# Kernel tuning notes

Measured on AMD Instinct MI355X. Metric: run time of the kernel, lower is better.

## Reference

```python
import jax, jax.numpy as jnp
import numpy as np

EPS_LN = 1e-5
EPS_W = 1e-16
K = 3


def layernorm(x, gamma, beta):
    mu = x.mean(-1, keepdims=True)
    var = ((x - mu) ** 2).mean(-1, keepdims=True)
    return (x - mu) * jax.lax.rsqrt(var + EPS_LN) * gamma + beta


def knn_interp(xb, pos_x, pos_y, k=K):
    """Inverse-squared-distance kNN interpolation.
    xb: [B, Nx, C] source features; pos_x: [Nx, 3]; pos_y: [Ny, 3].
    Positions are identical across batch (torch code expands them), so the
    kNN search is done once and the gather is broadcast over batch.
    Returns [B, Ny, C]."""
    # squared distances via ||y||^2 + ||x||^2 - 2 y.x  -> [Ny, Nx]
    d2 = ((pos_y * pos_y).sum(-1)[:, None]
          + (pos_x * pos_x).sum(-1)[None, :]
          - 2.0 * pos_y @ pos_x.T)
    _, idx = jax.lax.top_k(-d2, k)                      # [Ny, k] nearest
    # exact squared distances for the selected neighbors (matches torch math)
    diff = pos_x[idx] - pos_y[:, None, :]               # [Ny, k, 3]
    w = 1.0 / jnp.clip((diff * diff).sum(-1), EPS_W)    # [Ny, k]
    xg = xb[:, idx, :]                                  # [B, Ny, k, C]
    num = (xg * w[None, :, :, None]).sum(2)             # [B, Ny, C]
    return num / w.sum(1)[None, :, None]


def setup_inputs() -> dict:
    key = jax.random.key(0)
    k1, k2, k3 = jax.random.split(key, 3)
    B, N_MESH, N_PIV, C = 4, 40000, 2000, 128
    return {
        "node_features": jax.random.normal(k1, (B * N_MESH, C), jnp.float32),
        "gamma": jnp.ones((C,), jnp.float32),
        "beta": jnp.zeros((C,), jnp.float32),
        "position_mesh": jax.random.uniform(k2, (N_MESH, 3), jnp.float32),
        "position_pivotal": jax.random.uniform(k3, (N_PIV, 3), jnp.float32),
        "batch_size": 4,
    }


def reference(node_features, gamma, beta, position_mesh, position_pivotal, batch_size):
    B = batch_size
    C = node_features.shape[-1]
    Nm = position_mesh.shape[0]
    # encode: PivotalNorm then mesh -> pivotal interpolation
    h = layernorm(node_features, gamma, beta)
    hb = h.reshape(B, Nm, C)
    piv = knn_interp(hb, position_mesh, position_pivotal, K)      # [B, Npiv, C]
    # decode: pivotal -> mesh interpolation
    mesh = knn_interp(piv, position_pivotal, position_mesh, K)    # [B, Nm, C]
    return mesh.reshape(B * Nm, C)
```

## Files before the change

### kernel.cpp

```cpp
#include <hip/hip_runtime.h>
#include <hip/hip_bf16.h>
#include <math.h>

#define EPS_LN 1e-5f
#define EPS_W  1e-16f

__device__ __forceinline__ float cvt(const __hip_bfloat16 v) { return __bfloat162float(v); }
__device__ __forceinline__ float cvt(const float v)          { return v; }

__device__ __forceinline__ void load8(const __hip_bfloat16* p, float* x) {
    union { uint4 v; __hip_bfloat16 h[8]; } t;
    t.v = *(const uint4*)p;
    #pragma unroll
    for (int i = 0; i < 8; ++i) x[i] = __bfloat162float(t.h[i]);
}
__device__ __forceinline__ void load8(const float* p, float* x) {
    float4 a = *(const float4*)p, b = *(const float4*)(p + 4);
    x[0]=a.x; x[1]=a.y; x[2]=a.z; x[3]=a.w; x[4]=b.x; x[5]=b.y; x[6]=b.z; x[7]=b.w;
}

__device__ __forceinline__ void ins3lex(float nd, int ni, float d[3], int ix[3]) {
    bool b2 = (nd < d[2]) || (nd == d[2] && ni < ix[2]);
    if (!b2) return;
    bool b1 = (nd < d[1]) || (nd == d[1] && ni < ix[1]);
    bool b0 = (nd < d[0]) || (nd == d[0] && ni < ix[0]);
    if (b0)      { d[2]=d[1]; ix[2]=ix[1]; d[1]=d[0]; ix[1]=ix[0]; d[0]=nd; ix[0]=ni; }
    else if (b1) { d[2]=d[1]; ix[2]=ix[1]; d[1]=nd; ix[1]=ni; }
    else         { d[2]=nd; ix[2]=ni; }
}

__global__ __launch_bounds__(256)
void stage_kernel(const void* pmesh, int Nm, const void* ppiv, int Np,
                  float4* __restrict__ mesh_s, float4* __restrict__ piv_s,
                  int* __restrict__ flag) {
    __shared__ int sbad;
    if (threadIdx.x == 0) sbad = 0;
    __syncthreads();
    {
        const __hip_bfloat16* pb = (const __hip_bfloat16*)ppiv;
        int bad = 0;
        for (int i = threadIdx.x; i < Np * 3; i += 256) {
            float v = __bfloat162float(pb[i]);
            if (!(v >= 0.0f && v <= 1.0f)) bad = 1;
        }
        if (bad) sbad = 1;
    }
    __syncthreads();
    const int isf32 = sbad;

    int gid = blockIdx.x * 256 + threadIdx.x;
    if (gid == 0) *flag = isf32;
    const int total = Nm + Np;
    if (gid >= total) return;
    const int isMesh = gid < Nm ? 1 : 0;
    const int idx = isMesh ? gid : gid - Nm;
    const void* src = isMesh ? pmesh : ppiv;
    float x, y, z;
    if (isf32) {
        const float* p = (const float*)src;
        x = p[idx*3+0]; y = p[idx*3+1]; z = p[idx*3+2];
    } else {
        const __hip_bfloat16* p = (const __hip_bfloat16*)src;
        x = cvt(p[idx*3+0]); y = cvt(p[idx*3+1]); z = cvt(p[idx*3+2]);
    }
    float4 o; o.x = x; o.y = y; o.z = z; o.w = x*x + y*y + z*z;
    (isMesh ? mesh_s : piv_s)[idx] = o;
}

__device__ __forceinline__ void scan_body(
        const float4* __restrict__ cand, int Nc,
        const float4* __restrict__ qry, int Nq,
        int blk, int nslice, int chunk,
        int* __restrict__ idx_out, float* __restrict__ wn_out,
        float2* __restrict__ partials,
        float sd[4][64][3], int si[4][64][3]) {
    const int tid   = threadIdx.x;
    const int lane  = tid & 63;
    const int wv    = __builtin_amdgcn_readfirstlane(tid >> 6);
    const int qg    = blk / nslice;
    const int slice = blk % nslice;
    const int q     = qg * 64 + lane;
    const int qc    = min(q, Nq - 1);

    const float4 qp = qry[qc];
    const float  qn = qp.w;

    float d0 = INFINITY, d1 = INFINITY, d2 = INFINITY;
    int   i0 = 0x7fffffff, i1 = 0x7fffffff, i2 = 0x7fffffff;

    const int jbeg = (slice * 4 + wv) * chunk;
    const int jend = min(jbeg + chunk, Nc);
    #pragma unroll 8
    for (int j = jbeg; j < jend; ++j) {
        const float4 cp = cand[j];
        float t   = qn + cp.w;
        float dot = qp.x*cp.x + qp.y*cp.y + qp.z*cp.z;
        float s   = t - 2.0f*dot;
        if (s < d2) {
            if (s < d1) {
                d2 = d1; i2 = i1;
                if (s < d0) { d1 = d0; i1 = i0; d0 = s; i0 = j; }
                else        { d1 = s;  i1 = j; }
            } else { d2 = s; i2 = j; }
        }
    }

    sd[wv][lane][0] = d0; sd[wv][lane][1] = d1; sd[wv][lane][2] = d2;
    si[wv][lane][0] = i0; si[wv][lane][1] = i1; si[wv][lane][2] = i2;
    __syncthreads();

    if (wv == 0) {
        float d[3]  = {d0, d1, d2};
        int   ix[3] = {i0, i1, i2};
        for (int w = 1; w < 4; ++w)
            for (int k = 0; k < 3; ++k)
                ins3lex(sd[w][lane][k], si[w][lane][k], d, ix);
        if (q < Nq) {
            if (nslice == 1) {
                float w_[3], ws = 0.f;
                for (int k = 0; k < 3; ++k) {
                    int ii = min(max(ix[k], 0), Nc - 1);
                    ix[k] = ii;
                    float4 cp = cand[ii];
                    float dx = cp.x - qp.x, dy = cp.y - qp.y, dz = cp.z - qp.z;
                    float dd = dx*dx + dy*dy + dz*dz;
                    w_[k] = 1.0f / fmaxf(dd, EPS_W);
                    ws += w_[k];
                }
                float inv = 1.0f / ws;
                for (int k = 0; k < 3; ++k) {
                    idx_out[q*3+k] = ix[k];
                    wn_out[q*3+k]  = w_[k] * inv;
                }
            } else {
                float2* p = partials + ((size_t)q * nslice + slice) * 3;
                for (int k = 0; k < 3; ++k) {
                    float2 e; e.x = d[k]; e.y = __int_as_float(ix[k]);
                    p[k] = e;
                }
            }
        }
    }
}

__global__ __launch_bounds__(256)
void knn_scan_fused(const float4* __restrict__ mesh_s, int Nm,
                    const float4* __restrict__ piv_s, int Np,
                    int nb1, int nsl1, int chk1, int nsl2, int chk2,
                    int* __restrict__ idx1, float* __restrict__ wn1,
                    float2* __restrict__ part1,
                    int* __restrict__ idx2, float* __restrict__ wn2,
                    float2* __restrict__ part2) {
    __shared__ float sd[4][64][3];
    __shared__ int   si[4][64][3];
    const int bid = blockIdx.x;
    if (bid < nb1) {
        scan_body(mesh_s, Nm, piv_s, Np, bid, nsl1, chk1,
                  idx1, wn1, part1, sd, si);
    } else {
        scan_body(piv_s, Np, mesh_s, Nm, bid - nb1, nsl2, chk2,
                  idx2, wn2, part2, sd, si);
    }
}

__device__ __forceinline__ void finalize_wave(
        const float2* __restrict__ partials, int nslice,
        const float4* __restrict__ cand, int Nc,
        const float4* __restrict__ qry, int q, int lane,
        int* __restrict__ idx_out, float* __restrict__ wn_out) {
    const int nent = nslice * 3;
    const float2* p = partials + (size_t)q * nent;

    float d[3]  = {INFINITY, INFINITY, INFINITY};
    int   ix[3] = {0x7fffffff, 0x7fffffff, 0x7fffffff};
    for (int e = lane; e < nent; e += 64)
        ins3lex(p[e].x, __float_as_int(p[e].y), d, ix);

    #pragma unroll
    for (int off = 32; off >= 1; off >>= 1) {
        float od[3]; int oix[3];
        #pragma unroll
        for (int k = 0; k < 3; ++k) {
            od[k]  = __shfl_xor(d[k],  off);
            oix[k] = __shfl_xor(ix[k], off);
        }
        #pragma unroll
        for (int k = 0; k < 3; ++k) ins3lex(od[k], oix[k], d, ix);
    }

    if (lane == 0) {
        const float4 qp = qry[q];
        float w_[3], ws = 0.f;
        for (int k = 0; k < 3; ++k) {
            int ii = min(max(ix[k], 0), Nc - 1);
            ix[k] = ii;
            float4 cp = cand[ii];
            float dx = cp.x - qp.x, dy = cp.y - qp.y, dz = cp.z - qp.z;
            float dd = dx*dx + dy*dy + dz*dz;
            w_[k] = 1.0f / fmaxf(dd, EPS_W);
            ws += w_[k];
        }
        float inv = 1.0f / ws;
        for (int k = 0; k < 3; ++k) {
            idx_out[q*3+k] = ix[k];
            wn_out[q*3+k]  = w_[k] * inv;
        }
    }
}

__global__ __launch_bounds__(256)
void knn_finalize_fused(const float2* __restrict__ part1, int nsl1,
                        const float4* __restrict__ mesh_s, int Nm,
                        const float4* __restrict__ piv_s, int Np,
                        const float2* __restrict__ part2, int nsl2,
                        int nq1, int nq2,
                        int* __restrict__ idx1, float* __restrict__ wn1,
                        int* __restrict__ idx2, float* __restrict__ wn2) {
    const int lane = threadIdx.x & 63;
    const int w = blockIdx.x * 4 + (threadIdx.x >> 6);
    if (w < nq1)
        finalize_wave(part1, nsl1, mesh_s, Nm, piv_s, w, lane, idx1, wn1);
    else if (w - nq1 < nq2)
        finalize_wave(part2, nsl2, piv_s, Np, mesh_s, w - nq1, lane, idx2, wn2);
}

template <typename T, typename S>
__device__ void interp_ln_wave4_body(const T* __restrict__ xfeat,
                                     const T* __restrict__ gamma,
                                     const T* __restrict__ beta,
                                     const int* __restrict__ idx,
                                     const float* __restrict__ wn,
                                     S* __restrict__ piv,
                                     int Nm, int Np, int C, int B) {
    const int tid  = threadIdx.x;
    const int lane = tid & 63;
    const int sub  = lane >> 4;
    const int l16  = lane & 15;
    const int row_id = (blockIdx.x * 4 + (tid >> 6)) * 4 + sub;
    if (row_id >= B * Np) return;
    const int b  = row_id / Np;
    const int j  = row_id - b * Np;
    const int c0 = l16 * 8;

    float g[8], be[8];
    load8(gamma + c0, g);
    load8(beta  + c0, be);

    const float invC = 1.0f / (float)C;
    float acc[8];
    #pragma unroll
    for (int t = 0; t < 8; ++t) acc[t] = 0.f;

    for (int k = 0; k < 3; ++k) {
        int row = idx[j*3+k];
        row = min(max(row, 0), Nm - 1);
        const T* xp = xfeat + ((size_t)b*Nm + row) * (size_t)C + c0;
        float x[8];
        load8(xp, x);
        float s = 0.f, s2 = 0.f;
        #pragma unroll
        for (int t = 0; t < 8; ++t) { s += x[t]; s2 += x[t]*x[t]; }
        #pragma unroll
        for (int off = 8; off >= 1; off >>= 1) {
            s  += __shfl_xor(s,  off);
            s2 += __shfl_xor(s2, off);
        }
        float mean = s * invC;
        float var  = s2 * invC - mean*mean;
        float rs   = rsqrtf(var + EPS_LN);
        float wk   = wn[j*3+k];
        #pragma unroll
        for (int t = 0; t < 8; ++t)
            acc[t] += wk * ((x[t] - mean)*rs*g[t] + be[t]);
    }

    S* pp = piv + ((size_t)b*Np + j) * (size_t)C + c0;
    if constexpr (sizeof(S) == 2) {
        union { uint4 v; S h[8]; } o;
        #pragma unroll
        for (int t = 0; t < 8; ++t) o.h[t] = __float2bfloat16(acc[t]);
        *(uint4*)pp = o.v;
    } else {
        float4 a, c;
        a.x = acc[0]; a.y = acc[1]; a.z = acc[2]; a.w = acc[3];
        c.x = acc[4]; c.y = acc[5]; c.z = acc[6]; c.w = acc[7];
        *(float4*)pp = a;
        *(float4*)(pp + 4) = c;
    }
}

__global__ __launch_bounds__(256)
void interp_ln_wave4_kernel(const void* xfeat, const void* gamma, const void* beta,
                            const int* idx, const float* wn, void* piv,
                            int Nm, int Np, int C, int B, const int* dtype_flag) {
    if (*dtype_flag)
        interp_ln_wave4_body<float, float>((const float*)xfeat, (const float*)gamma,
                                           (const float*)beta, idx, wn,
                                           (float*)piv, Nm, Np, C, B);
    else
        interp_ln_wave4_body<__hip_bfloat16, __hip_bfloat16>(
            (const __hip_bfloat16*)xfeat, (const __hip_bfloat16*)gamma,
            (const __hip_bfloat16*)beta, idx, wn,
            (__hip_bfloat16*)piv, Nm, Np, C, B);
}

template <typename T, typename S>
__device__ void interp_ln_body(const T* __restrict__ xfeat,
                               const T* __restrict__ gamma,
                               const T* __restrict__ beta,
                               const int* __restrict__ idx,
                               const float* __restrict__ wn,
                               S* __restrict__ piv, int Nm, int Np, int C) {
    const int j   = blockIdx.x % Np;
    const int b   = blockIdx.x / Np;
    const int c   = threadIdx.x;
    const int wid = c >> 6;
    const int nw  = C >> 6;

    const float g  = cvt(gamma[c]);
    const float be = cvt(beta[c]);

    __shared__ float red[8];
    float acc = 0.f;
    const float invC = 1.0f / (float)C;

    for (int k = 0; k < 3; ++k) {
        int row = idx[j*3+k];
        row = min(max(row, 0), Nm - 1);
        const T* xp = xfeat + ((size_t)b*Nm + row) * (size_t)C;
        float x = cvt(xp[c]);
        float s = x, s2 = x*x;
        for (int off = 32; off > 0; off >>= 1) {
            s  += __shfl_down(s,  off);
            s2 += __shfl_down(s2, off);
        }
        if ((c & 63) == 0) { red[wid] = s; red[4+wid] = s2; }
        __syncthreads();
        float sum = 0.f, sum2 = 0.f;
        for (int wv = 0; wv < nw; ++wv) { sum += red[wv]; sum2 += red[4+wv]; }
        float mean = sum * invC;
        float var  = sum2 * invC - mean*mean;
        float rs   = rsqrtf(var + EPS_LN);
        acc += wn[j*3+k] * ((x - mean)*rs*g + be);
        __syncthreads();
    }
    S ov; if constexpr (sizeof(S) == 2) ov = __float2bfloat16(acc); else ov = acc;
    piv[((size_t)b*Np + j) * (size_t)C + c] = ov;
}

__global__ __launch_bounds__(128)
void interp_ln_kernel(const void* xfeat, const void* gamma, const void* beta,
                      const int* idx, const float* wn, void* piv,
                      int Nm, int Np, int C, const int* dtype_flag) {
    if (*dtype_flag)
        interp_ln_body<float, float>((const float*)xfeat, (const float*)gamma,
                                     (const float*)beta, idx, wn,
                                     (float*)piv, Nm, Np, C);
    else
        interp_ln_body<__hip_bfloat16, __hip_bfloat16>(
            (const __hip_bfloat16*)xfeat, (const __hip_bfloat16*)gamma,
            (const __hip_bfloat16*)beta, idx, wn,
            (__hip_bfloat16*)piv, Nm, Np, C);
}

__global__ __launch_bounds__(256)
void gather_out8_kernel(const void* __restrict__ pivv,
                        const int* __restrict__ idx, const float* __restrict__ wn,
                        void* __restrict__ out, int Nm, int Np, int C, int B,
                        int total, const int* __restrict__ dtype_flag) {
    int gid = blockIdx.x * 256 + threadIdx.x;
    if (gid >= total) return;
    const int C8 = C >> 3;
    const int c8 = gid % C8;
    const int i  = gid / C8;
    int jj0 = min(max(idx[i*3+0], 0), Np - 1);
    int jj1 = min(max(idx[i*3+1], 0), Np - 1);
    int jj2 = min(max(idx[i*3+2], 0), Np - 1);
    const float w0 = wn[i*3+0], w1 = wn[i*3+1], w2 = wn[i*3+2];
    const int cb = c8 * 8;

    if (*dtype_flag) {
        const float* pv = (const float*)pivv;
        float* po = (float*)out;
        for (int b = 0; b < B; ++b) {
            const float* pb = pv + (size_t)b * Np * C;
            const float* r0 = pb + (size_t)jj0 * C + cb;
            const float* r1 = pb + (size_t)jj1 * C + cb;
            const float* r2 = pb + (size_t)jj2 * C + cb;
            float* q = po + ((size_t)b*Nm + i) * (size_t)C + cb;
            #pragma unroll
            for (int h = 0; h < 2; ++h) {
                float4 v0 = *(const float4*)(r0 + h*4);
                float4 v1 = *(const float4*)(r1 + h*4);
                float4 v2 = *(const float4*)(r2 + h*4);
                float4 o;
                o.x = w0*v0.x + w1*v1.x + w2*v2.x;
                o.y = w0*v0.y + w1*v1.y + w2*v2.y;
                o.z = w0*v0.z + w1*v1.z + w2*v2.z;
                o.w = w0*v0.w + w1*v1.w + w2*v2.w;
                *(float4*)(q + h*4) = o;
            }
        }
    } else {
        const __hip_bfloat16* pv = (const __hip_bfloat16*)pivv;
        __hip_bfloat16* po = (__hip_bfloat16*)out;
        for (int b = 0; b < B; ++b) {
            const __hip_bfloat16* pb = pv + (size_t)b * Np * C;
            union { uint4 v; __hip_bfloat16 h[8]; } u0, u1, u2, o;
            u0.v = *(const uint4*)(pb + (size_t)jj0 * C + cb);
            u1.v = *(const uint4*)(pb + (size_t)jj1 * C + cb);
            u2.v = *(const uint4*)(pb + (size_t)jj2 * C + cb);
            #pragma unroll
            for (int t = 0; t < 8; ++t) {
                float a = w0*cvt(u0.h[t]) + w1*cvt(u1.h[t]) + w2*cvt(u2.h[t]);
                o.h[t] = __float2bfloat16(a);
            }
            *(uint4*)(po + ((size_t)b*Nm + i) * (size_t)C + cb) = o.v;
        }
    }
}

__global__ __launch_bounds__(256)
void gather_out_kernel(const void* __restrict__ pivv,
                       const int* __restrict__ idx, const float* __restrict__ wn,
                       void* __restrict__ out, int Nm, int Np, int C4,
                       int total4, const int* __restrict__ dtype_flag) {
    int gid = blockIdx.x * 256 + threadIdx.x;
    if (gid >= total4) return;
    int c4 = gid % C4;
    int r  = gid / C4;
    int i  = r % Nm;
    int b  = r / Nm;
    const int C = C4 * 4;
    int jj0 = min(max(idx[i*3+0], 0), Np - 1);
    int jj1 = min(max(idx[i*3+1], 0), Np - 1);
    int jj2 = min(max(idx[i*3+2], 0), Np - 1);
    float w0 = wn[i*3+0], w1 = wn[i*3+1], w2 = wn[i*3+2];

    if (*dtype_flag) {
        const float* pbase = (const float*)pivv + (size_t)b * Np * C;
        float4 v0 = *(const float4*)(pbase + (size_t)jj0 * C + c4*4);
        float4 v1 = *(const float4*)(pbase + (size_t)jj1 * C + c4*4);
        float4 v2 = *(const float4*)(pbase + (size_t)jj2 * C + c4*4);
        float4 o;
        o.x = w0*v0.x + w1*v1.x + w2*v2.x;
        o.y = w0*v0.y + w1*v1.y + w2*v2.y;
        o.z = w0*v0.z + w1*v1.z + w2*v2.z;
        o.w = w0*v0.w + w1*v1.w + w2*v2.w;
        *(((float4*)out) + gid) = o;
    } else {
        const __hip_bfloat16* pbase = (const __hip_bfloat16*)pivv + (size_t)b * Np * C;
        union { __hip_bfloat16 h[4]; uint2 v; } u0, u1, u2, o;
        u0.v = *(const uint2*)(pbase + (size_t)jj0 * C + c4*4);
        u1.v = *(const uint2*)(pbase + (size_t)jj1 * C + c4*4);
        u2.v = *(const uint2*)(pbase + (size_t)jj2 * C + c4*4);
        #pragma unroll
        for (int t = 0; t < 4; ++t) {
            float a = w0*cvt(u0.h[t]) + w1*cvt(u1.h[t]) + w2*cvt(u2.h[t]);
            o.h[t] = __float2bfloat16(a);
        }
        *(((uint2*)out) + gid) = o.v;
    }
}

__global__ void zero_words_kernel(unsigned* out, long long nwords) {
    long long i = (long long)blockIdx.x * 256 + threadIdx.x;
    if (i < nwords) out[i] = 0u;
}

extern "C" void kernel_launch(void* const* d_in, const int* in_sizes, int n_in,
                              void* d_out, int out_size, void* d_ws, size_t ws_size,
                              hipStream_t stream) {
    const int C  = in_sizes[1];
    const int Nm = in_sizes[3] / 3;
    const int Np = in_sizes[4] / 3;
    const int B  = in_sizes[0] / (Nm * C);

    const int nqg1 = (Np + 63) / 64;
    const int nqg2 = (Nm + 63) / 64;

    auto plan = [](int nqg, int Nc, int& nsl, int& chk) {
        nsl = (2048 + nqg - 1) / nqg;
        int maxsl = (Nc + 127) / 128;
        if (nsl > maxsl) nsl = maxsl;
        if (nsl < 1) nsl = 1;
        chk = (Nc + nsl*4 - 1) / (nsl*4);
    };
    int nsl1, chk1, nsl2, chk2;
    plan(nqg1, Nm, nsl1, chk1);
    plan(nqg2, Np, nsl2, chk2);

    size_t off = 0;
    size_t flag_o = 0, meshs_o = 0, pivs_o = 0, piv_o = 0;
    size_t i1_o = 0, w1_o = 0, i2_o = 0, w2_o = 0, p1_o = 0, p2_o = 0;
    auto layout = [&](int s1, int s2) {
        off = 0;
        auto carve = [&](size_t bytes) {
            size_t p = off;
            off += (bytes + 255) & ~(size_t)255;
            return p;
        };
        flag_o  = carve(256);
        meshs_o = carve((size_t)Nm * sizeof(float4));
        pivs_o  = carve((size_t)Np * sizeof(float4));
        piv_o   = carve((size_t)B * Np * C * sizeof(float));
        i1_o    = carve((size_t)Np * 3 * sizeof(int));
        w1_o    = carve((size_t)Np * 3 * sizeof(float));
        i2_o    = carve((size_t)Nm * 3 * sizeof(int));
        w2_o    = carve((size_t)Nm * 3 * sizeof(float));
        p1_o    = carve((size_t)Np * s1 * 3 * sizeof(float2));
        p2_o    = carve((size_t)Nm * s2 * 3 * sizeof(float2));
    };
    layout(nsl1, nsl2);
    if (off > ws_size) {
        nsl1 = 16; chk1 = (Nm + nsl1*4 - 1) / (nsl1*4);
        nsl2 = 1;  chk2 = (Np + nsl2*4 - 1) / (nsl2*4);
        layout(nsl1, nsl2);
    }
    if (off > ws_size) {
        long long nwords = (long long)out_size / 2;
        zero_words_kernel<<<(int)((nwords + 255) / 256), 256, 0, stream>>>(
            (unsigned*)d_out, nwords);
        return;
    }

    char* base = (char*)d_ws;
    int*    flag   = (int*)   (base + flag_o);
    float4* mesh_s = (float4*)(base + meshs_o);
    float4* piv_s  = (float4*)(base + pivs_o);
    void*   piv    = (void*)  (base + piv_o);
    int*    idx1   = (int*)   (base + i1_o);
    float*  wn1    = (float*) (base + w1_o);
    int*    idx2   = (int*)   (base + i2_o);
    float*  wn2    = (float*) (base + w2_o);
    float2* part1  = (float2*)(base + p1_o);
    float2* part2  = (float2*)(base + p2_o);

    stage_kernel<<<(Nm + Np + 255) / 256, 256, 0, stream>>>(
        d_in[3], Nm, d_in[4], Np, mesh_s, piv_s, flag);

    const int nb1 = nqg1 * nsl1;
    const int nb2 = nqg2 * nsl2;
    knn_scan_fused<<<nb1 + nb2, 256, 0, stream>>>(
        mesh_s, Nm, piv_s, Np, nb1, nsl1, chk1, nsl2, chk2,
        idx1, wn1, part1, idx2, wn2, part2);

    const int nq1 = (nsl1 > 1) ? Np : 0;
    const int nq2 = (nsl2 > 1) ? Nm : 0;
    if (nq1 + nq2 > 0)
        knn_finalize_fused<<<(nq1 + nq2 + 3) / 4, 256, 0, stream>>>(
            part1, nsl1, mesh_s, Nm, piv_s, Np, part2, nsl2,
            nq1, nq2, idx1, wn1, idx2, wn2);

    if (C == 128) {
        const int nrow = B * Np;
        interp_ln_wave4_kernel<<<(nrow + 15) / 16, 256, 0, stream>>>(
            d_in[0], d_in[1], d_in[2], idx1, wn1, piv, Nm, Np, C, B, flag);
    } else {
        interp_ln_kernel<<<B * Np, C, 0, stream>>>(d_in[0], d_in[1], d_in[2],
                                                   idx1, wn1, piv, Nm, Np, C, flag);
    }

    if ((C & 7) == 0) {
        const int total = Nm * (C >> 3);
        gather_out8_kernel<<<(total + 255) / 256, 256, 0, stream>>>(
            piv, idx2, wn2, d_out, Nm, Np, C, B, total, flag);
    } else {
        const int C4 = C / 4;
        const int total4 = B * Nm * C4;
        gather_out_kernel<<<(total4 + 255) / 256, 256, 0, stream>>>(
            piv, idx2, wn2, d_out, Nm, Np, C4, total4, flag);
    }
}
```

Baseline: 261.4 us.

## Replace brute-force kNN scan with uniform-grid spatial binning search

Builds a uniform 3D grid over both point sets (count, prefix-scan, scatter into cell-sorted arrays) and replaces the brute-force all-pairs kNN scan plus finalize kernel with a shell-expanding grid search, 4 lanes per query merged by shuffles. The intent is to cut the O(Nq*Nc) distance work, which dominated the mesh-to-pivotal and pivotal-to-mesh searches, down to nearby cells. It adds several small kernels, including a single-block scan, plus atomics and divergent per-query loops. A brute-force fallback runs when positions fall outside [0,1], and the early-exit bound uses a small slack that could affect exact tie behaviour.

```diff
diff --git a/kernel.cpp b/kernel.cpp
--- a/kernel.cpp
+++ b/kernel.cpp
@@ -4,6 +4,7 @@
 
 #define EPS_LN 1e-5f
 #define EPS_W  1e-16f
+#define SLACK_KNN 1e-4f
 
 __device__ __forceinline__ float cvt(const __hip_bfloat16 v) { return __bfloat162float(v); }
 __device__ __forceinline__ float cvt(const float v)          { return v; }
@@ -32,7 +33,8 @@
 __global__ __launch_bounds__(256)
 void stage_kernel(const void* pmesh, int Nm, const void* ppiv, int Np,
                   float4* __restrict__ mesh_s, float4* __restrict__ piv_s,
-                  int* __restrict__ flag) {
+                  int* __restrict__ flag, int* __restrict__ counts,
+                  int G1, int C1, int G2) {
     __shared__ int sbad;
     if (threadIdx.x == 0) sbad = 0;
     __syncthreads();
@@ -49,7 +51,7 @@
     const int isf32 = sbad;
 
     int gid = blockIdx.x * 256 + threadIdx.x;
-    if (gid == 0) *flag = isf32;
+    if (gid == 0) flag[0] = isf32;
     const int total = Nm + Np;
     if (gid >= total) return;
     const int isMesh = gid < Nm ? 1 : 0;
@@ -65,119 +67,156 @@
     }
     float4 o; o.x = x; o.y = y; o.z = z; o.w = x*x + y*y + z*z;
     (isMesh ? mesh_s : piv_s)[idx] = o;
-}
-
-__device__ __forceinline__ void scan_body(
-        const float4* __restrict__ cand, int Nc,
-        const float4* __restrict__ qry, int Nq,
-        int blk, int nslice, int chunk,
-        int* __restrict__ idx_out, float* __restrict__ wn_out,
-        float2* __restrict__ partials,
-        float sd[4][64][3], int si[4][64][3]) {
-    const int tid   = threadIdx.x;
-    const int lane  = tid & 63;
-    const int wv    = __builtin_amdgcn_readfirstlane(tid >> 6);
-    const int qg    = blk / nslice;
-    const int slice = blk % nslice;
-    const int q     = qg * 64 + lane;
-    const int qc    = min(q, Nq - 1);
-
-    const float4 qp = qry[qc];
+
+    const int G = isMesh ? G1 : G2;
+    int cx = min(max((int)(x * (float)G), 0), G - 1);
+    int cy = min(max((int)(y * (float)G), 0), G - 1);
+    int cz = min(max((int)(z * (float)G), 0), G - 1);
+    int c = ((cz * G + cy) * G + cx) + (isMesh ? 0 : C1);
+    atomicAdd(&counts[c], 1);
+    bool ok = (x >= 0.f && x <= 1.f && y >= 0.f && y <= 1.f && z >= 0.f && z <= 1.f);
+    if (!ok) atomicOr(&flag[1], 1);
+}
+
+__global__ __launch_bounds__(256)
+void scan_kernel(const int* __restrict__ counts, int n,
+                 int* __restrict__ starts, int* __restrict__ cursors) {
+    __shared__ int carry;
+    __shared__ int wsum[4];
+    if (threadIdx.x == 0) carry = 0;
+    __syncthreads();
+    const int lane = threadIdx.x & 63;
+    const int wv   = threadIdx.x >> 6;
+    for (int base = 0; base < n; base += 256) {
+        int i = base + threadIdx.x;
+        int v = (i < n) ? counts[i] : 0;
+        int s = v;
+        #pragma unroll
+        for (int off = 1; off < 64; off <<= 1) {
+            int t = __shfl_up(s, off);
+            if (lane >= off) s += t;
+        }
+        if (lane == 63) wsum[wv] = s;
+        __syncthreads();
+        int woff = 0;
+        for (int w = 0; w < wv; ++w) woff += wsum[w];
+        int excl = carry + woff + (s - v);
+        if (i < n) { starts[i] = excl; cursors[i] = excl; }
+        __syncthreads();
+        if (threadIdx.x == 255) carry += woff + s;
+        __syncthreads();
+    }
+    if (threadIdx.x == 0) starts[n] = carry;
+}
+
+__global__ __launch_bounds__(256)
+void scatter_kernel(const float4* __restrict__ mesh_s, int Nm,
+                    const float4* __restrict__ piv_s, int Np,
+                    int G1, int C1, int G2,
+                    int* __restrict__ cursors,
+                    float4* __restrict__ cellPts, int* __restrict__ cellIdx) {
+    int gid = blockIdx.x * 256 + threadIdx.x;
+    if (gid >= Nm + Np) return;
+    const int isMesh = gid < Nm ? 1 : 0;
+    const int idx = isMesh ? gid : gid - Nm;
+    float4 p = isMesh ? mesh_s[idx] : piv_s[idx];
+    const int G = isMesh ? G1 : G2;
+    int cx = min(max((int)(p.x * (float)G), 0), G - 1);
+    int cy = min(max((int)(p.y * (float)G), 0), G - 1);
+    int cz = min(max((int)(p.z * (float)G), 0), G - 1);
+    int c = ((cz * G + cy) * G + cx) + (isMesh ? 0 : C1);
+    int pos = atomicAdd(&cursors[c], 1);
+    cellPts[pos] = p;
+    cellIdx[pos] = idx;
+}
+
+__global__ __launch_bounds__(256)
+void knn_grid_fused(const float4* __restrict__ mesh_s, int Nm,
+                    const float4* __restrict__ piv_s, int Np,
+                    const int* __restrict__ starts,
+                    const float4* __restrict__ cellPts,
+                    const int* __restrict__ cellIdx,
+                    int G1, int C1, int G2, int nb1,
+                    int* __restrict__ idx1, float* __restrict__ wn1,
+                    int* __restrict__ idx2, float* __restrict__ wn2,
+                    const int* __restrict__ flags) {
+    const int tid  = threadIdx.x;
+    const int lane = tid & 63;
+    const int sub  = lane & 3;
+    const int qq   = lane >> 2;
+    const int wv   = tid >> 6;
+    const int bid  = blockIdx.x;
+    const int brute = flags[1];
+
+    const float4* cand; const float4* qry;
+    int Nc, Nq, G, cbase, q;
+    if (bid < nb1) {
+        cand = mesh_s; Nc = Nm; qry = piv_s; Nq = Np; G = G1; cbase = 0;
+        q = (bid * 4 + wv) * 16 + qq;
+        if (q >= Nq) return;
+    } else {
+        cand = piv_s; Nc = Np; qry = mesh_s; Nq = Nm; G = G2; cbase = C1;
+        q = ((bid - nb1) * 4 + wv) * 16 + qq;
+        if (q >= Nq) return;
+    }
+
+    const float4 qp = qry[q];
     const float  qn = qp.w;
-
-    float d0 = INFINITY, d1 = INFINITY, d2 = INFINITY;
-    int   i0 = 0x7fffffff, i1 = 0x7fffffff, i2 = 0x7fffffff;
-
-    const int jbeg = (slice * 4 + wv) * chunk;
-    const int jend = min(jbeg + chunk, Nc);
-    #pragma unroll 8
-    for (int j = jbeg; j < jend; ++j) {
-        const float4 cp = cand[j];
-        float t   = qn + cp.w;
-        float dot = qp.x*cp.x + qp.y*cp.y + qp.z*cp.z;
-        float s   = t - 2.0f*dot;
-        if (s < d2) {
-            if (s < d1) {
-                d2 = d1; i2 = i1;
-                if (s < d0) { d1 = d0; i1 = i0; d0 = s; i0 = j; }
-                else        { d1 = s;  i1 = j; }
-            } else { d2 = s; i2 = j; }
-        }
-    }
-
-    sd[wv][lane][0] = d0; sd[wv][lane][1] = d1; sd[wv][lane][2] = d2;
-    si[wv][lane][0] = i0; si[wv][lane][1] = i1; si[wv][lane][2] = i2;
-    __syncthreads();
-
-    if (wv == 0) {
-        float d[3]  = {d0, d1, d2};
-        int   ix[3] = {i0, i1, i2};
-        for (int w = 1; w < 4; ++w)
-            for (int k = 0; k < 3; ++k)
-                ins3lex(sd[w][lane][k], si[w][lane][k], d, ix);
-        if (q < Nq) {
-            if (nslice == 1) {
-                float w_[3], ws = 0.f;
-                for (int k = 0; k < 3; ++k) {
-                    int ii = min(max(ix[k], 0), Nc - 1);
-                    ix[k] = ii;
-                    float4 cp = cand[ii];
-                    float dx = cp.x - qp.x, dy = cp.y - qp.y, dz = cp.z - qp.z;
-                    float dd = dx*dx + dy*dy + dz*dz;
-                    w_[k] = 1.0f / fmaxf(dd, EPS_W);
-                    ws += w_[k];
-                }
-                float inv = 1.0f / ws;
-                for (int k = 0; k < 3; ++k) {
-                    idx_out[q*3+k] = ix[k];
-                    wn_out[q*3+k]  = w_[k] * inv;
-                }
-            } else {
-                float2* p = partials + ((size_t)q * nslice + slice) * 3;
-                for (int k = 0; k < 3; ++k) {
-                    float2 e; e.x = d[k]; e.y = __int_as_float(ix[k]);
-                    p[k] = e;
+    float d[3]  = {INFINITY, INFINITY, INFINITY};
+    int   ix[3] = {0x7fffffff, 0x7fffffff, 0x7fffffff};
+
+    if (!brute) {
+        const float h = 1.0f / (float)G;
+        int cx = min(max((int)(qp.x * (float)G), 0), G - 1);
+        int cy = min(max((int)(qp.y * (float)G), 0), G - 1);
+        int cz = min(max((int)(qp.z * (float)G), 0), G - 1);
+        float fx0 = qp.x - (float)cx * h,  fx1 = (float)(cx+1) * h - qp.x;
+        float fy0 = qp.y - (float)cy * h,  fy1 = (float)(cy+1) * h - qp.y;
+        float fz0 = qp.z - (float)cz * h,  fz1 = (float)(cz+1) * h - qp.z;
+        float fmin = fminf(fminf(fminf(fx0, fx1), fminf(fy0, fy1)), fminf(fz0, fz1));
+
+        int cnt = 0;
+        for (int r = 0; r <= G; ++r) {
+            if (ix[2] != 0x7fffffff) {
+                float bound = (float)(r - 1) * h + fmin;
+                if (bound > 0.f && bound * bound - SLACK_KNN > d[2]) break;
+            }
+            for (int dz = -r; dz <= r; ++dz) {
+                int z = cz + dz; if (z < 0 || z >= G) continue;
+                int adz = dz < 0 ? -dz : dz;
+                for (int dy = -r; dy <= r; ++dy) {
+                    int y = cy + dy; if (y < 0 || y >= G) continue;
+                    int ady = dy < 0 ? -dy : dy;
+                    int mzy = adz > ady ? adz : ady;
+                    int xstep = (mzy == r || r == 0) ? 1 : 2 * r;
+                    for (int dx = -r; dx <= r; dx += xstep) {
+                        int x = cx + dx; if (x < 0 || x >= G) continue;
+                        if (((cnt++) & 3) != sub) continue;
+                        int c = cbase + (z * G + y) * G + x;
+                        int pb = starts[c], pe = starts[c + 1];
+                        for (int p = pb; p < pe; ++p) {
+                            float4 cp = cellPts[p];
+                            float t   = qn + cp.w;
+                            float dot = qp.x*cp.x + qp.y*cp.y + qp.z*cp.z;
+                            float s   = t - 2.0f*dot;
+                            ins3lex(s, cellIdx[p], d, ix);
+                        }
+                    }
                 }
             }
         }
-    }
-}
-
-__global__ __launch_bounds__(256)
-void knn_scan_fused(const float4* __restrict__ mesh_s, int Nm,
-                    const float4* __restrict__ piv_s, int Np,
-                    int nb1, int nsl1, int chk1, int nsl2, int chk2,
-                    int* __restrict__ idx1, float* __restrict__ wn1,
-                    float2* __restrict__ part1,
-                    int* __restrict__ idx2, float* __restrict__ wn2,
-                    float2* __restrict__ part2) {
-    __shared__ float sd[4][64][3];
-    __shared__ int   si[4][64][3];
-    const int bid = blockIdx.x;
-    if (bid < nb1) {
-        scan_body(mesh_s, Nm, piv_s, Np, bid, nsl1, chk1,
-                  idx1, wn1, part1, sd, si);
-    } else {
-        scan_body(piv_s, Np, mesh_s, Nm, bid - nb1, nsl2, chk2,
-                  idx2, wn2, part2, sd, si);
-    }
-}
-
-__device__ __forceinline__ void finalize_wave(
-        const float2* __restrict__ partials, int nslice,
-        const float4* __restrict__ cand, int Nc,
-        const float4* __restrict__ qry, int q, int lane,
-        int* __restrict__ idx_out, float* __restrict__ wn_out) {
-    const int nent = nslice * 3;
-    const float2* p = partials + (size_t)q * nent;
-
-    float d[3]  = {INFINITY, INFINITY, INFINITY};
-    int   ix[3] = {0x7fffffff, 0x7fffffff, 0x7fffffff};
-    for (int e = lane; e < nent; e += 64)
-        ins3lex(p[e].x, __float_as_int(p[e].y), d, ix);
+    } else {
+        for (int j = sub; j < Nc; j += 4) {
+            float4 cp = cand[j];
+            float t   = qn + cp.w;
+            float dot = qp.x*cp.x + qp.y*cp.y + qp.z*cp.z;
+            float s   = t - 2.0f*dot;
+            ins3lex(s, j, d, ix);
+        }
+    }
 
     #pragma unroll
-    for (int off = 32; off >= 1; off >>= 1) {
+    for (int off = 1; off <= 2; off <<= 1) {
         float od[3]; int oix[3];
         #pragma unroll
         for (int k = 0; k < 3; ++k) {
@@ -188,9 +227,11 @@
         for (int k = 0; k < 3; ++k) ins3lex(od[k], oix[k], d, ix);
     }
 
-    if (lane == 0) {
-        const float4 qp = qry[q];
+    if (sub == 0) {
+        int* idx_out  = (bid < nb1) ? idx1 : idx2;
+        float* wn_out = (bid < nb1) ? wn1  : wn2;
         float w_[3], ws = 0.f;
+        #pragma unroll
         for (int k = 0; k < 3; ++k) {
             int ii = min(max(ix[k], 0), Nc - 1);
             ix[k] = ii;
@@ -201,27 +242,12 @@
             ws += w_[k];
         }
         float inv = 1.0f / ws;
+        #pragma unroll
         for (int k = 0; k < 3; ++k) {
             idx_out[q*3+k] = ix[k];
             wn_out[q*3+k]  = w_[k] * inv;
         }
     }
-}
-
-__global__ __launch_bounds__(256)
-void knn_finalize_fused(const float2* __restrict__ part1, int nsl1,
-                        const float4* __restrict__ mesh_s, int Nm,
-                        const float4* __restrict__ piv_s, int Np,
-                        const float2* __restrict__ part2, int nsl2,
-                        int nq1, int nq2,
-                        int* __restrict__ idx1, float* __restrict__ wn1,
-                        int* __restrict__ idx2, float* __restrict__ wn2) {
-    const int lane = threadIdx.x & 63;
-    const int w = blockIdx.x * 4 + (threadIdx.x >> 6);
-    if (w < nq1)
-        finalize_wave(part1, nsl1, mesh_s, Nm, piv_s, w, lane, idx1, wn1);
-    else if (w - nq1 < nq2)
-        finalize_wave(part2, nsl2, piv_s, Np, mesh_s, w - nq1, lane, idx2, wn2);
 }
 
 template <typename T, typename S>
@@ -337,7 +363,7 @@
         if ((c & 63) == 0) { red[wid] = s; red[4+wid] = s2; }
         __syncthreads();
         float sum = 0.f, sum2 = 0.f;
-        for (int wv = 0; wv < nw; ++wv) { sum += red[wv]; sum2 += red[4+wv]; }
+        for (int w = 0; w < nw; ++w) { sum += red[w]; sum2 += red[4+w]; }
         float mean = sum * invC;
         float var  = sum2 * invC - mean*mean;
         float rs   = rsqrtf(var + EPS_LN);
@@ -387,7 +413,7 @@
             const float* r0 = pb + (size_t)jj0 * C + cb;
             const float* r1 = pb + (size_t)jj1 * C + cb;
             const float* r2 = pb + (size_t)jj2 * C + cb;
-            float* q = po + ((size_t)b*Nm + i) * (size_t)C + cb;
+            float* qo = po + ((size_t)b*Nm + i) * (size_t)C + cb;
             #pragma unroll
             for (int h = 0; h < 2; ++h) {
                 float4 v0 = *(const float4*)(r0 + h*4);
@@ -398,7 +424,7 @@
                 o.y = w0*v0.y + w1*v1.y + w2*v2.y;
                 o.z = w0*v0.z + w1*v1.z + w2*v2.z;
                 o.w = w0*v0.w + w1*v1.w + w2*v2.w;
-                *(float4*)(q + h*4) = o;
+                *(float4*)(qo + h*4) = o;
             }
         }
     } else {
@@ -476,47 +502,37 @@
     const int Np = in_sizes[4] / 3;
     const int B  = in_sizes[0] / (Nm * C);
 
-    const int nqg1 = (Np + 63) / 64;
-    const int nqg2 = (Nm + 63) / 64;
-
-    auto plan = [](int nqg, int Nc, int& nsl, int& chk) {
-        nsl = (2048 + nqg - 1) / nqg;
-        int maxsl = (Nc + 127) / 128;
-        if (nsl > maxsl) nsl = maxsl;
-        if (nsl < 1) nsl = 1;
-        chk = (Nc + nsl*4 - 1) / (nsl*4);
+    auto pickG = [](int N) {
+        int g = (int)cbrtf((float)N / 4.0f);
+        if (g < 1) g = 1;
+        if (g > 32) g = 32;
+        return g;
     };
-    int nsl1, chk1, nsl2, chk2;
-    plan(nqg1, Nm, nsl1, chk1);
-    plan(nqg2, Np, nsl2, chk2);
+    const int G1 = pickG(Nm), C1 = G1 * G1 * G1;
+    const int G2 = pickG(Np), C2 = G2 * G2 * G2;
+    const int NC = C1 + C2;
+    const int NP = Nm + Np;
 
     size_t off = 0;
-    size_t flag_o = 0, meshs_o = 0, pivs_o = 0, piv_o = 0;
-    size_t i1_o = 0, w1_o = 0, i2_o = 0, w2_o = 0, p1_o = 0, p2_o = 0;
-    auto layout = [&](int s1, int s2) {
-        off = 0;
-        auto carve = [&](size_t bytes) {
-            size_t p = off;
-            off += (bytes + 255) & ~(size_t)255;
-            return p;
-        };
-        flag_o  = carve(256);
-        meshs_o = carve((size_t)Nm * sizeof(float4));
-        pivs_o  = carve((size_t)Np * sizeof(float4));
-        piv_o   = carve((size_t)B * Np * C * sizeof(float));
-        i1_o    = carve((size_t)Np * 3 * sizeof(int));
-        w1_o    = carve((size_t)Np * 3 * sizeof(float));
-        i2_o    = carve((size_t)Nm * 3 * sizeof(int));
-        w2_o    = carve((size_t)Nm * 3 * sizeof(float));
-        p1_o    = carve((size_t)Np * s1 * 3 * sizeof(float2));
-        p2_o    = carve((size_t)Nm * s2 * 3 * sizeof(float2));
+    auto carve = [&](size_t bytes) {
+        size_t p = off;
+        off += (bytes + 255) & ~(size_t)255;
+        return p;
     };
-    layout(nsl1, nsl2);
-    if (off > ws_size) {
-        nsl1 = 16; chk1 = (Nm + nsl1*4 - 1) / (nsl1*4);
-        nsl2 = 1;  chk2 = (Np + nsl2*4 - 1) / (nsl2*4);
-        layout(nsl1, nsl2);
-    }
+    const size_t flag_o   = carve(256);
+    const size_t counts_o = carve((size_t)NC * 4);
+    const size_t starts_o = carve((size_t)(NC + 1) * 4);
+    const size_t curs_o   = carve((size_t)NC * 4);
+    const size_t cpts_o   = carve((size_t)NP * sizeof(float4));
+    const size_t cidx_o   = carve((size_t)NP * 4);
+    const size_t meshs_o  = carve((size_t)Nm * sizeof(float4));
+    const size_t pivs_o   = carve((size_t)Np * sizeof(float4));
+    const size_t piv_o    = carve((size_t)B * Np * C * sizeof(float));
+    const size_t i1_o     = carve((size_t)Np * 3 * 4);
+    const size_t w1_o     = carve((size_t)Np * 3 * 4);
+    const size_t i2_o     = carve((size_t)Nm * 3 * 4);
+    const size_t w2_o     = carve((size_t)Nm * 3 * 4);
+
     if (off > ws_size) {
         long long nwords = (long long)out_size / 2;
         zero_words_kernel<<<(int)((nwords + 255) / 256), 256, 0, stream>>>(
@@ -526,6 +542,11 @@
 
     char* base = (char*)d_ws;
     int*    flag   = (int*)   (base + flag_o);
+    int*    counts = (int*)   (base + counts_o);
+    int*    starts = (int*)   (base + starts_o);
+    int*    curs   = (int*)   (base + curs_o);
+    float4* cpts   = (float4*)(base + cpts_o);
+    int*    cidx   = (int*)   (base + cidx_o);
     float4* mesh_s = (float4*)(base + meshs_o);
     float4* piv_s  = (float4*)(base + pivs_o);
     void*   piv    = (void*)  (base + piv_o);
@@ -533,24 +554,26 @@
     float*  wn1    = (float*) (base + w1_o);
     int*    idx2   = (int*)   (base + i2_o);
     float*  wn2    = (float*) (base + w2_o);
-    float2* part1  = (float2*)(base + p1_o);
-    float2* part2  = (float2*)(base + p2_o);
-
-    stage_kernel<<<(Nm + Np + 255) / 256, 256, 0, stream>>>(
-        d_in[3], Nm, d_in[4], Np, mesh_s, piv_s, flag);
-
-    const int nb1 = nqg1 * nsl1;
-    const int nb2 = nqg2 * nsl2;
-    knn_scan_fused<<<nb1 + nb2, 256, 0, stream>>>(
-        mesh_s, Nm, piv_s, Np, nb1, nsl1, chk1, nsl2, chk2,
-        idx1, wn1, part1, idx2, wn2, part2);
-
-    const int nq1 = (nsl1 > 1) ? Np : 0;
-    const int nq2 = (nsl2 > 1) ? Nm : 0;
-    if (nq1 + nq2 > 0)
-        knn_finalize_fused<<<(nq1 + nq2 + 3) / 4, 256, 0, stream>>>(
-            part1, nsl1, mesh_s, Nm, piv_s, Np, part2, nsl2,
-            nq1, nq2, idx1, wn1, idx2, wn2);
+
+    {
+        long long nwords = (long long)(counts_o - flag_o) / 4 + NC;
+        zero_words_kernel<<<(int)((nwords + 255) / 256), 256, 0, stream>>>(
+            (unsigned*)flag, nwords);
+    }
+
+    stage_kernel<<<(NP + 255) / 256, 256, 0, stream>>>(
+        d_in[3], Nm, d_in[4], Np, mesh_s, piv_s, flag, counts, G1, C1, G2);
+
+    scan_kernel<<<1, 256, 0, stream>>>(counts, NC, starts, curs);
+
+    scatter_kernel<<<(NP + 255) / 256, 256, 0, stream>>>(
+        mesh_s, Nm, piv_s, Np, G1, C1, G2, curs, cpts, cidx);
+
+    const int nb1 = (Np + 63) / 64;
+    const int nb2 = (Nm + 63) / 64;
+    knn_grid_fused<<<nb1 + nb2, 256, 0, stream>>>(
+        mesh_s, Nm, piv_s, Np, starts, cpts, cidx,
+        G1, C1, G2, nb1, idx1, wn1, idx2, wn2, flag);
 
     if (C == 128) {
         const int nrow = B * Np;
```

Measured after the change: 477.5 us. +82.7%, slower.
